# Performance work log

Hardware: AMD Instinct MI355X
Metric: run time of the kernel (lower is better)

## Reference

```python
import jax, jax.numpy as jnp
import numpy as np

EMBED = 64
HEADS = 2
HDIM = EMBED // HEADS  # 32
IN_FEAT = 256
NODES = 3


def _lin(x, W, b=None):
    y = x @ W.T
    return y + b if b is not None else y


def setup_inputs() -> dict:
    key = jax.random.key(0)
    ks = jax.random.split(key, 24)
    B = 131072
    s = 0.05
    inp = {
        "spatial": jax.random.normal(ks[0], (B, IN_FEAT), jnp.float32),
        "genomic": jax.random.normal(ks[1], (B, IN_FEAT), jnp.float32),
        "temporal": jax.random.normal(ks[2], (B, IN_FEAT), jnp.float32),
        "adj_matrix": jnp.ones((B, NODES, NODES), jnp.float32),
        # modality projections (Linear(256,64))
        "Wsp": jax.random.normal(ks[3], (EMBED, IN_FEAT)) * s,
        "bsp": jnp.zeros((EMBED,)),
        "Wge": jax.random.normal(ks[4], (EMBED, IN_FEAT)) * s,
        "bge": jnp.zeros((EMBED,)),
        "Wtm": jax.random.normal(ks[5], (EMBED, IN_FEAT)) * s,
        "btm": jnp.zeros((EMBED,)),
        # GAT: W Linear(64,64,no bias), attention Linear(2*head_dim=64 -> 1, no bias)
        "gat_W": jax.random.normal(ks[6], (EMBED, EMBED)) * s,
        "gat_a": jax.random.normal(ks[7], (2 * HDIM,)) * s,
        # MultiheadAttention(64, 2)
        "in_w": jax.random.normal(ks[8], (3 * EMBED, EMBED)) * s,
        "in_b": jnp.zeros((3 * EMBED,)),
        "out_w": jax.random.normal(ks[9], (EMBED, EMBED)) * s,
        "out_b": jnp.zeros((EMBED,)),
        # LayerNorm(64)
        "ln_g": jnp.ones((EMBED,)),
        "ln_b": jnp.zeros((EMBED,)),
        # predictor 64->32->16->2
        "p1_w": jax.random.normal(ks[10], (32, EMBED)) * s,
        "p1_b": jnp.zeros((32,)),
        "p2_w": jax.random.normal(ks[11], (16, 32)) * s,
        "p2_b": jnp.zeros((16,)),
        "p3_w": jax.random.normal(ks[12], (2, 16)) * s,
        "p3_b": jnp.zeros((2,)),
    }
    return inp


def reference(spatial, genomic, temporal, adj_matrix,
              Wsp, bsp, Wge, bge, Wtm, btm,
              gat_W, gat_a, in_w, in_b, out_w, out_b,
              ln_g, ln_b, p1_w, p1_b, p2_w, p2_b, p3_w, p3_b):
    # Dropout layers are identity in eval mode.
    B = spatial.shape[0]
    sp = jax.nn.relu(_lin(spatial, Wsp, bsp))   # [B, 64]
    ge = jax.nn.relu(_lin(genomic, Wge, bge))
    tm = jax.nn.relu(_lin(temporal, Wtm, btm))
    x = jnp.stack([sp, ge, tm], axis=1)          # [B, 3, 64]

    # ---- GAT layer (dense attention over 3 nodes, 2 heads) ----
    h = _lin(x, gat_W).reshape(B, NODES, HEADS, HDIM)  # [B,3,H,D]
    # a . concat(h_i, h_j) decomposes into a1.h_i + a2.h_j
    e_i = jnp.einsum('bnhd,d->bnh', h, gat_a[:HDIM])
    e_j = jnp.einsum('bnhd,d->bnh', h, gat_a[HDIM:])
    e = e_i[:, :, None, :] + e_j[:, None, :, :]        # [B,3,3,H]
    e = jnp.where(e > 0, e, 0.2 * e)                    # LeakyReLU(0.2)
    e = jnp.where(adj_matrix[..., None] == 0, -1e9, e)
    alpha = jax.nn.softmax(e, axis=2)                   # softmax over j
    h_out = jnp.einsum('bijh,bjhd->bihd', alpha, h).reshape(B, NODES, EMBED)
    gat_pooled = h_out.mean(axis=1)                     # [B, 64]

    # ---- Cross-modal MHA + residual LayerNorm ----
    qkv = _lin(x, in_w, in_b)                           # [B,3,192]
    q, k, v = jnp.split(qkv, 3, axis=-1)
    def heads(t):
        return t.reshape(B, NODES, HEADS, HDIM).transpose(0, 2, 1, 3)
    q, k, v = heads(q), heads(k), heads(v)              # [B,H,3,D]
    sc = jnp.einsum('bhqd,bhkd->bhqk', q, k) / jnp.sqrt(jnp.float32(HDIM))
    attn = jax.nn.softmax(sc, axis=-1)
    o = jnp.einsum('bhqk,bhkd->bhqd', attn, v).transpose(0, 2, 1, 3).reshape(B, NODES, EMBED)
    attn_out = _lin(o, out_w, out_b)
    y = x + attn_out
    mu = y.mean(-1, keepdims=True)
    var = ((y - mu) ** 2).mean(-1, keepdims=True)
    y = (y - mu) / jnp.sqrt(var + 1e-5) * ln_g + ln_b
    cross_modal = y.mean(axis=1)                        # [B, 64]

    # ---- Predictor ----
    combined = gat_pooled + cross_modal
    z = jax.nn.relu(_lin(combined, p1_w, p1_b))
    z = jax.nn.relu(_lin(z, p2_w, p2_b))
    out = _lin(z, p3_w, p3_b)                           # [B, 2]
    return out[:, 0], out[:, 1]
```

## Files before the change

### kernel.cpp

```cpp
#include <hip/hip_runtime.h>

typedef __attribute__((ext_vector_type(8))) short v8s;
typedef __attribute__((ext_vector_type(4))) float v4f;

#define MFMA16(a, b, c) __builtin_amdgcn_mfma_f32_16x16x32_bf16((a), (b), (c), 0, 0, 0)
#define SCQ 0.17677669529663687f

__device__ __forceinline__ short f2bf(float f) {
    unsigned u = __float_as_uint(f);
    u += 0x7FFFu + ((u >> 16) & 1u);
    return (short)(u >> 16);
}
__device__ __forceinline__ float bf2f(short s) {
    return __uint_as_float(((unsigned)(unsigned short)s) << 16);
}
__device__ __forceinline__ float bfly16(float v) {
#pragma unroll
    for (int m = 1; m < 16; m <<= 1) v += __shfl_xor(v, m);
    return v;
}
__device__ __forceinline__ void gload16(const float* g, float* l) {
    __builtin_amdgcn_global_load_lds((const __attribute__((address_space(1))) void*)g,
                                     (__attribute__((address_space(3))) void*)l, 16, 0, 0);
}

__global__ void giman_prep(const float* __restrict__ Wsp, const float* __restrict__ Wge,
                           const float* __restrict__ Wtm, const float* __restrict__ gatW,
                           const float* __restrict__ gat_a,
                           const float* __restrict__ inw, const float* __restrict__ outw,
                           const float* __restrict__ p1w, const float* __restrict__ p2w,
                           const float* __restrict__ in_b, const float* __restrict__ out_b,
                           short* __restrict__ ws) {
    int idx = blockIdx.x * 256 + threadIdx.x;
    if (idx < 73216) {
        int j = idx & 7, l = (idx >> 3) & 63;
        int lr = l & 15, lc = ((l >> 4) << 3) + j;
        float val;
        if (idx < 49152) {
            const float* W; int off;
            if (idx < 16384)      { W = Wsp; off = idx; }
            else if (idx < 32768) { W = Wge; off = idx - 16384; }
            else                  { W = Wtm; off = idx - 32768; }
            int t = off >> 9, kk = t & 7, nb = t >> 3;
            val = W[(nb * 16 + lr) * 256 + kk * 32 + lc];
        } else if (idx < 54272) {
            int t = (idx - 49152) >> 9, kk = t & 1, nb = t >> 1;
            if (nb < 4) {
                val = gatW[(nb * 16 + lr) * 64 + kk * 32 + lc];
            } else {
                int f = kk * 32 + lc;
                val = 0.f;
                if (lr < 4) {
                    float s = 0.f;
                    for (int d = 0; d < 32; ++d)
                        s += gat_a[(lr >> 1) * 32 + d] * gatW[((lr & 1) * 32 + d) * 64 + f];
                    val = s;
                } else if (lr < 6) {
                    int h = lr - 4;
                    float s = 0.f;
                    for (int d = 0; d < 32; ++d)
                        s += inw[(32 * h + d) * 64 + f] * in_b[64 + 32 * h + d];
                    val = s * SCQ;
                } else if (lr < 8) {
                    int h = lr - 6;
                    float s = 0.f;
                    for (int d = 0; d < 32; ++d)
                        s += inw[(64 + 32 * h + d) * 64 + f] * in_b[32 * h + d];
                    val = s * SCQ;
                }
            }
        } else if (idx < 62464) {
            int t = (idx - 54272) >> 9, kk = t & 1, nbh = t >> 1;
            int h = nbh >> 2, nb = nbh & 3;
            int a = kk * 32 + lc, b = nb * 16 + lr;
            float s = 0.f;
            for (int d = 0; d < 32; ++d)
                s += inw[(32 * h + d) * 64 + a] * inw[(64 + 32 * h + d) * 64 + b];
            val = s * SCQ;
        } else if (idx < 70656) {
            int t = (idx - 62464) >> 9, kk = t & 1, nbh = t >> 1;
            int h = nbh >> 2, nb = nbh & 3;
            int r = nb * 16 + lr, c = kk * 32 + lc;
            float s = 0.f;
            for (int k = 0; k < 32; ++k)
                s += outw[r * 64 + h * 32 + k] * inw[(128 + h * 32 + k) * 64 + c];
            val = s;
        } else if (idx < 72704) {
            int t = (idx - 70656) >> 9, kk = t & 1, nb = t >> 1;
            val = p1w[(nb * 16 + lr) * 64 + kk * 32 + lc];
        } else {
            val = p2w[lr * 32 + lc];
        }
        ws[idx] = f2bf(val);
    } else if (idx < 73280) {
        int r = idx - 73216;
        float s = out_b[r];
        for (int k = 0; k < 64; ++k) s += outw[r * 64 + 128 + k] * in_b[128 + k];
        ((float*)(ws + 73216))[r] = s;
    } else if (idx < 73282) {
        int h = idx - 73280;
        float s = 0.f;
        for (int d = 0; d < 32; ++d) s += in_b[32 * h + d] * in_b[64 + 32 * h + d];
        ((float*)(ws + 73216))[64 + h] = s * SCQ;
    }
}

__global__ __launch_bounds__(256)
void giman_proj(const float* __restrict__ spatial, const float* __restrict__ genomic,
                const float* __restrict__ temporal,
                const float* __restrict__ bsp, const float* __restrict__ bge,
                const float* __restrict__ btm,
                const short* __restrict__ wf, short* __restrict__ xg, int Btot)
{
    __shared__ __align__(16) float xs[32][260];

    const int wv = threadIdx.x >> 6;
    const int lane = threadIdx.x & 63;
    const int lq = lane & 15, lg = lane >> 4;
    const int half = wv & 1;
    const int nbp  = wv >> 1;
    const int nG = Btot >> 5;
    const int nItems = 3 * nG;

    for (int it = blockIdx.x; it < nItems; it += gridDim.x) {
        const int m = it / nG;
        const int g = it - m * nG;
        const int s0 = g * 32;

        const float* Xm = (m == 0 ? spatial : (m == 1 ? genomic : temporal));
        const float* src = Xm + (size_t)s0 * 256;
        const float* Bm = (m == 0 ? bsp : (m == 1 ? bge : btm));
        const v8s* bwf = (const v8s*)(wf + m * 16384);

#pragma unroll
        for (int i = 0; i < 8; ++i) {
            int row = wv * 8 + i;
            gload16(src + row * 256 + lane * 4, &xs[row][0]);
        }
        __syncthreads();

        v4f acc0 = (v4f){0.f, 0.f, 0.f, 0.f};
        v4f acc1 = (v4f){0.f, 0.f, 0.f, 0.f};
#pragma unroll
        for (int kk = 0; kk < 8; ++kk) {
            const float* rp = &xs[half * 16 + lq][kk * 32 + lg * 8];
            float4 u = *(const float4*)rp;
            float4 v = *(const float4*)(rp + 4);
            v8s af;
            af[0] = f2bf(u.x); af[1] = f2bf(u.y); af[2] = f2bf(u.z); af[3] = f2bf(u.w);
            af[4] = f2bf(v.x); af[5] = f2bf(v.y); af[6] = f2bf(v.z); af[7] = f2bf(v.w);
            acc0 = MFMA16(af, bwf[((nbp * 2 + 0) * 8 + kk) * 64 + lane], acc0);
            acc1 = MFMA16(af, bwf[((nbp * 2 + 1) * 8 + kk) * 64 + lane], acc1);
        }

        float bb0 = Bm[nbp * 32 + lq], bb1 = Bm[nbp * 32 + 16 + lq];
#pragma unroll
        for (int r = 0; r < 4; ++r) {
            int row = s0 + half * 16 + 4 * lg + r;
            size_t base = ((size_t)row * 3 + m) * 64 + nbp * 32 + lq;
            float v0 = acc0[r] + bb0; v0 = v0 > 0.f ? v0 : 0.f;
            float v1 = acc1[r] + bb1; v1 = v1 > 0.f ? v1 : 0.f;
            xg[base] = f2bf(v0);
            xg[base + 16] = f2bf(v1);
        }
        __syncthreads();
    }
}

__global__ __launch_bounds__(256)
void giman_main(const float* __restrict__ adj, const short* __restrict__ wf,
                const short* __restrict__ xg,
                const float* __restrict__ ln_g, const float* __restrict__ ln_b,
                const float* __restrict__ p1b, const float* __restrict__ p2b,
                const float* __restrict__ p3w, const float* __restrict__ p3bb,
                float* __restrict__ dout, int Btot)
{
    __shared__ __align__(16) short x_lds[4][48][72];
    __shared__ __align__(16) short v_lds[4][16][72];
    __shared__ __align__(16) float a_lds[4][148];

    const int wv   = threadIdx.x >> 6;
    const int lane = threadIdx.x & 63;
    const int lq   = lane & 15;
    const int lg   = lane >> 4;
    const int grpb = lane & 48;
    const int s0   = blockIdx.x * 64 + wv * 16;
    if (s0 + 16 > Btot) return;

    short (*xw)[72] = x_lds[wv];
    short (*vtr)[72] = v_lds[wv];

    if (lane < 36)
        *(float4*)&a_lds[wv][lane * 4] = *(const float4*)(adj + (size_t)s0 * 9 + lane * 4);

    {
        const short* xsrc = xg + (size_t)s0 * 192;
#pragma unroll
        for (int i = 0; i < 6; ++i) {
            int c = lane + 64 * i;
            v8s val = *(const v8s*)(xsrc + c * 8);
            *(v8s*)&xw[c >> 3][(c & 7) * 8] = val;
        }
    }

    const float* cbp = (const float*)(wf + 73216);
    float cbv[4], lgv[4], lbv[4];
#pragma unroll
    for (int nb = 0; nb < 4; ++nb) {
        int c = nb * 16 + lq;
        cbv[nb] = cbp[c];
        lgv[nb] = ln_g[c];
        lbv[nb] = ln_b[c];
    }
    const float gmv0 = cbp[64], gmv1 = cbp[65];
    const float inv3 = 1.f / 3.f;

    const v8s* gwf = (const v8s*)(wf + 49152);
    const v8s* pff = (const v8s*)(wf + 54272);
    const v8s* uf  = (const v8s*)(wf + 62464);

#pragma unroll 1
    for (int t = 0; t < 4; ++t) {
        int rn = lq & 3; rn = (rn == 3) ? 2 : rn;
        const short* xrp = xw[(t * 4 + (lq >> 2)) * 3 + rn];
        v8s xa0 = *(const v8s*)(xrp + lg * 8);
        v8s xa1 = *(const v8s*)(xrp + 32 + lg * 8);

        float gp[4];
        v4f eacc = (v4f){0.f, 0.f, 0.f, 0.f};
        {
            v4f hacc[4];
#pragma unroll
            for (int nb = 0; nb < 4; ++nb) {
                v4f a = (v4f){0.f, 0.f, 0.f, 0.f};
                a = MFMA16(xa0, gwf[(nb * 2 + 0) * 64 + lane], a);
                a = MFMA16(xa1, gwf[(nb * 2 + 1) * 64 + lane], a);
                hacc[nb] = a;
            }
            eacc = MFMA16(xa0, gwf[8 * 64 + lane], eacc);
            eacc = MFMA16(xa1, gwf[9 * 64 + lane], eacc);

            const float* amp = &a_lds[wv][(t * 4 + lg) * 9];
            float wj0[2], wj1[2], wj2[2];
#pragma unroll
            for (int h = 0; h < 2; ++h) {
                float ei0 = __shfl(eacc[0], grpb + h);
                float ei1 = __shfl(eacc[1], grpb + h);
                float ei2 = __shfl(eacc[2], grpb + h);
                float ej0 = __shfl(eacc[0], grpb + 2 + h);
                float ej1 = __shfl(eacc[1], grpb + 2 + h);
                float ej2 = __shfl(eacc[2], grpb + 2 + h);
                float w0 = 0.f, w1 = 0.f, w2 = 0.f;
#pragma unroll
                for (int i = 0; i < 3; ++i) {
                    float eiv = i == 0 ? ei0 : (i == 1 ? ei1 : ei2);
                    float e0 = eiv + ej0; e0 = e0 > 0.f ? e0 : 0.2f * e0; if (amp[i * 3 + 0] == 0.f) e0 = -1e9f;
                    float e1 = eiv + ej1; e1 = e1 > 0.f ? e1 : 0.2f * e1; if (amp[i * 3 + 1] == 0.f) e1 = -1e9f;
                    float e2 = eiv + ej2; e2 = e2 > 0.f ? e2 : 0.2f * e2; if (amp[i * 3 + 2] == 0.f) e2 = -1e9f;
                    float mx = fmaxf(e0, fmaxf(e1, e2));
                    float q0 = __expf(e0 - mx), q1 = __expf(e1 - mx), q2 = __expf(e2 - mx);
                    float inv = 1.f / (q0 + q1 + q2);
                    w0 += q0 * inv; w1 += q1 * inv; w2 += q2 * inv;
                }
                wj0[h] = w0; wj1[h] = w1; wj2[h] = w2;
            }
#pragma unroll
            for (int nb = 0; nb < 4; ++nb) {
                int h = nb >> 1;
                gp[nb] = (wj0[h] * hacc[nb][0] + wj1[h] * hacc[nb][1] + wj2[h] * hacc[nb][2]) * inv3;
            }
        }

        float y[4][3];
#pragma unroll
        for (int nb = 0; nb < 4; ++nb)
#pragma unroll
            for (int r = 0; r < 3; ++r)
                y[nb][r] = bf2f(xw[(t * 4 + lg) * 3 + r][nb * 16 + lq]) + cbv[nb];

        const int sb = grpb + (grpb >> 2);
#pragma unroll
        for (int h = 0; h < 2; ++h) {
            {
                v4f va[4];
#pragma unroll
                for (int nb = 0; nb < 4; ++nb) {
                    v4f a = (v4f){0.f, 0.f, 0.f, 0.f};
                    a = MFMA16(xa0, pff[((h * 4 + nb) * 2 + 0) * 64 + lane], a);
                    a = MFMA16(xa1, pff[((h * 4 + nb) * 2 + 1) * 64 + lane], a);
                    va[nb] = a;
                }
#pragma unroll
                for (int nb = 0; nb < 4; ++nb)
#pragma unroll
                    for (int r = 0; r < 3; ++r)
                        vtr[lg * 4 + r][nb * 16 + lq] = f2bf(va[nb][r]);
            }
            v8s aq0 = *(const v8s*)&vtr[lq][lg * 8];
            v8s aq1 = *(const v8s*)&vtr[lq][32 + lg * 8];
            v4f S = (v4f){0.f, 0.f, 0.f, 0.f};
            S = MFMA16(aq0, xa0, S);
            S = MFMA16(aq1, xa1, S);

            float alh[9];
            {
                float gm = h ? gmv1 : gmv0;
                float bv0 = __shfl(eacc[0], grpb + 6 + h) + gm;
                float bv1 = __shfl(eacc[1], grpb + 6 + h) + gm;
                float bv2 = __shfl(eacc[2], grpb + 6 + h) + gm;
#pragma unroll
                for (int i = 0; i < 3; ++i) {
                    float av = __shfl(eacc[i], grpb + 4 + h);
                    float e0 = __shfl(S[i], sb + 0) + av + bv0;
                    float e1 = __shfl(S[i], sb + 1) + av + bv1;
                    float e2 = __shfl(S[i], sb + 2) + av + bv2;
                    float mx = fmaxf(e0, fmaxf(e1, e2));
                    float w0 = __expf(e0 - mx), w1 = __expf(e1 - mx), w2 = __expf(e2 - mx);
                    float inv = 1.f / (w0 + w1 + w2);
                    alh[i * 3 + 0] = w0 * inv;
                    alh[i * 3 + 1] = w1 * inv;
                    alh[i * 3 + 2] = w2 * inv;
                }
            }

#pragma unroll
            for (int nb = 0; nb < 4; ++nb) {
                v4f u = (v4f){0.f, 0.f, 0.f, 0.f};
                u = MFMA16(xa0, uf[((h * 4 + nb) * 2 + 0) * 64 + lane], u);
                u = MFMA16(xa1, uf[((h * 4 + nb) * 2 + 1) * 64 + lane], u);
#pragma unroll
                for (int r = 0; r < 3; ++r)
                    y[nb][r] += alh[r * 3 + 0] * u[0] + alh[r * 3 + 1] * u[1]
                              + alh[r * 3 + 2] * u[2];
            }
        }

        float mu[3], rs[3];
#pragma unroll
        for (int r = 0; r < 3; ++r) {
            float sm = y[0][r] + y[1][r] + y[2][r] + y[3][r];
            float sq = y[0][r] * y[0][r] + y[1][r] * y[1][r]
                     + y[2][r] * y[2][r] + y[3][r] * y[3][r];
            sm = bfly16(sm); sq = bfly16(sq);
            float m_ = sm * (1.f / 64.f);
            float var = sq * (1.f / 64.f) - m_ * m_;
            mu[r] = m_;
            rs[r] = rsqrtf(var + 1e-5f);
        }
#pragma unroll
        for (int nb = 0; nb < 4; ++nb) {
            float cm = (y[nb][0] - mu[0]) * rs[0] + (y[nb][1] - mu[1]) * rs[1]
                     + (y[nb][2] - mu[2]) * rs[2];
            float comb = gp[nb] + cm * inv3 * lgv[nb] + lbv[nb];
            xw[t * 4 + lg][nb * 16 + lq] = f2bf(comb);
        }
    }

    {
        const v8s* p1f = (const v8s*)(wf + 70656);
        const v8s* p2f = (const v8s*)(wf + 72704);
        short (*zw)[40] = (short (*)[40])(&xw[16][0]);
        const short* crp = &xw[lq][0];
        v8s ca0 = *(const v8s*)(crp + lg * 8);
        v8s ca1 = *(const v8s*)(crp + 32 + lg * 8);
        const float pb1v0 = p1b[lq], pb1v1 = p1b[16 + lq], pb2v = p2b[lq];
        const float p3w0 = p3w[lq], p3w1 = p3w[16 + lq];
        v4f z1[2];
#pragma unroll
        for (int nb = 0; nb < 2; ++nb) {
            float bb = nb ? pb1v1 : pb1v0;
            v4f a = (v4f){bb, bb, bb, bb};
            a = MFMA16(ca0, p1f[(nb * 2 + 0) * 64 + lane], a);
            a = MFMA16(ca1, p1f[(nb * 2 + 1) * 64 + lane], a);
            z1[nb] = a;
        }
#pragma unroll
        for (int nb = 0; nb < 2; ++nb)
#pragma unroll
            for (int r = 0; r < 4; ++r) {
                float v = z1[nb][r];
                v = v > 0.f ? v : 0.f;
                zw[lg * 4 + r][nb * 16 + lq] = f2bf(v);
            }
        v8s za = *(const v8s*)(&zw[lq][0] + lg * 8);
        v4f z2 = (v4f){pb2v, pb2v, pb2v, pb2v};
        z2 = MFMA16(za, p2f[lane], z2);
        const float p3b0 = p3bb[0], p3b1 = p3bb[1];
#pragma unroll
        for (int r = 0; r < 4; ++r) {
            float v = z2[r];
            v = v > 0.f ? v : 0.f;
            float po0 = bfly16(v * p3w0);
            float po1 = bfly16(v * p3w1);
            if (lq == 0) {
                dout[s0 + lg * 4 + r] = po0 + p3b0;
                dout[Btot + s0 + lg * 4 + r] = po1 + p3b1;
            }
        }
    }
}

extern "C" void kernel_launch(void* const* d_in, const int* in_sizes, int n_in,
                              void* d_out, int out_size, void* d_ws, size_t ws_size,
                              hipStream_t stream) {
    const float* spatial  = (const float*)d_in[0];
    const float* genomic  = (const float*)d_in[1];
    const float* temporal = (const float*)d_in[2];
    const float* adj      = (const float*)d_in[3];
    const float* Wsp = (const float*)d_in[4];
    const float* bsp = (const float*)d_in[5];
    const float* Wge = (const float*)d_in[6];
    const float* bge = (const float*)d_in[7];
    const float* Wtm = (const float*)d_in[8];
    const float* btm = (const float*)d_in[9];
    const float* gatW  = (const float*)d_in[10];
    const float* gat_a = (const float*)d_in[11];
    const float* in_w  = (const float*)d_in[12];
    const float* in_b  = (const float*)d_in[13];
    const float* out_w = (const float*)d_in[14];
    const float* out_b = (const float*)d_in[15];
    const float* ln_g  = (const float*)d_in[16];
    const float* ln_b  = (const float*)d_in[17];
    const float* p1w = (const float*)d_in[18];
    const float* p1b = (const float*)d_in[19];
    const float* p2w = (const float*)d_in[20];
    const float* p2b = (const float*)d_in[21];
    const float* p3w = (const float*)d_in[22];
    const float* p3b = (const float*)d_in[23];
    float* out = (float*)d_out;
    const int Btot = in_sizes[0] / 256;

    short* wf = (short*)d_ws;
    short* xg = wf + 81920;

    giman_prep<<<(73282 + 255) / 256, 256, 0, stream>>>(Wsp, Wge, Wtm, gatW, gat_a,
                                                        in_w, out_w, p1w, p2w,
                                                        in_b, out_b, wf);
    giman_proj<<<1024, 256, 0, stream>>>(spatial, genomic, temporal,
                                         bsp, bge, btm, wf, xg, Btot);
    giman_main<<<Btot / 64, 256, 0, stream>>>(adj, wf, xg,
                                              ln_g, ln_b, p1b, p2b, p3w, p3b,
                                              out, Btot);
}
```

Measured before the change: 221.3 us.

## Double-buffer projection input loads with async LDS prefetch and per-modality grid

The projection kernel now processes 16-row tiles with double-buffered LDS, issuing the global-to-LDS loads for the next tile before computing the current one and using explicit vmcnt waits instead of full syncs. Each block is pinned to one modality through blockIdx.y, and each wave computes one 16-column output block instead of two. The grid becomes 342x3 blocks. The aim is to hide HBM latency on a bandwidth-bound projection, at the cost of fragile hand-counted waitcnt logic and less MFMA work per wave.

```diff
diff --git a/kernel.cpp b/kernel.cpp
--- a/kernel.cpp
+++ b/kernel.cpp
@@ -112,58 +112,64 @@
                 const float* __restrict__ btm,
                 const short* __restrict__ wf, short* __restrict__ xg, int Btot)
 {
-    __shared__ __align__(16) float xs[32][260];
+    __shared__ __align__(16) float xs[2][16][260];
 
     const int wv = threadIdx.x >> 6;
     const int lane = threadIdx.x & 63;
     const int lq = lane & 15, lg = lane >> 4;
-    const int half = wv & 1;
-    const int nbp  = wv >> 1;
-    const int nG = Btot >> 5;
-    const int nItems = 3 * nG;
-
-    for (int it = blockIdx.x; it < nItems; it += gridDim.x) {
-        const int m = it / nG;
-        const int g = it - m * nG;
-        const int s0 = g * 32;
-
-        const float* Xm = (m == 0 ? spatial : (m == 1 ? genomic : temporal));
-        const float* src = Xm + (size_t)s0 * 256;
-        const float* Bm = (m == 0 ? bsp : (m == 1 ? bge : btm));
-        const v8s* bwf = (const v8s*)(wf + m * 16384);
-
-#pragma unroll
-        for (int i = 0; i < 8; ++i) {
-            int row = wv * 8 + i;
-            gload16(src + row * 256 + lane * 4, &xs[row][0]);
-        }
-        __syncthreads();
-
-        v4f acc0 = (v4f){0.f, 0.f, 0.f, 0.f};
-        v4f acc1 = (v4f){0.f, 0.f, 0.f, 0.f};
+    const int m = blockIdx.y;
+    const int nG = Btot >> 4;
+
+    const float* Xm = (m == 0 ? spatial : (m == 1 ? genomic : temporal));
+    const float* Bm = (m == 0 ? bsp : (m == 1 ? bge : btm));
+    const v8s* bwf = (const v8s*)(wf + m * 16384);
+    const float bb = Bm[wv * 16 + lq];
+
+    const int g0 = blockIdx.x;
+    const int nit = (nG - g0 + gridDim.x - 1) / gridDim.x;
+
+    {
+        const float* src = Xm + (size_t)g0 * 16 * 256;
+#pragma unroll
+        for (int i = 0; i < 4; ++i)
+            gload16(src + (wv * 4 + i) * 256 + lane * 4, &xs[0][wv * 4 + i][0]);
+    }
+
+    for (int it = 0; it < nit; ++it) {
+        const int cur = it & 1;
+        if (it + 1 < nit) {
+            const float* src = Xm + ((size_t)g0 + (size_t)(it + 1) * gridDim.x) * 16 * 256;
+#pragma unroll
+            for (int i = 0; i < 4; ++i)
+                gload16(src + (wv * 4 + i) * 256 + lane * 4, &xs[cur ^ 1][wv * 4 + i][0]);
+            if (it == 0) { asm volatile("s_waitcnt vmcnt(4)" ::: "memory"); }
+            else         { asm volatile("s_waitcnt vmcnt(8)" ::: "memory"); }
+        } else {
+            asm volatile("s_waitcnt vmcnt(4)" ::: "memory");
+        }
+        __builtin_amdgcn_sched_barrier(0);
+        __builtin_amdgcn_s_barrier();
+
+        v4f acc = (v4f){0.f, 0.f, 0.f, 0.f};
 #pragma unroll
         for (int kk = 0; kk < 8; ++kk) {
-            const float* rp = &xs[half * 16 + lq][kk * 32 + lg * 8];
+            const float* rp = &xs[cur][lq][kk * 32 + lg * 8];
             float4 u = *(const float4*)rp;
             float4 v = *(const float4*)(rp + 4);
             v8s af;
             af[0] = f2bf(u.x); af[1] = f2bf(u.y); af[2] = f2bf(u.z); af[3] = f2bf(u.w);
             af[4] = f2bf(v.x); af[5] = f2bf(v.y); af[6] = f2bf(v.z); af[7] = f2bf(v.w);
-            acc0 = MFMA16(af, bwf[((nbp * 2 + 0) * 8 + kk) * 64 + lane], acc0);
-            acc1 = MFMA16(af, bwf[((nbp * 2 + 1) * 8 + kk) * 64 + lane], acc1);
-        }
-
-        float bb0 = Bm[nbp * 32 + lq], bb1 = Bm[nbp * 32 + 16 + lq];
+            acc = MFMA16(af, bwf[(wv * 8 + kk) * 64 + lane], acc);
+        }
+
+        const int s0 = (g0 + it * gridDim.x) * 16;
 #pragma unroll
         for (int r = 0; r < 4; ++r) {
-            int row = s0 + half * 16 + 4 * lg + r;
-            size_t base = ((size_t)row * 3 + m) * 64 + nbp * 32 + lq;
-            float v0 = acc0[r] + bb0; v0 = v0 > 0.f ? v0 : 0.f;
-            float v1 = acc1[r] + bb1; v1 = v1 > 0.f ? v1 : 0.f;
-            xg[base] = f2bf(v0);
-            xg[base + 16] = f2bf(v1);
-        }
-        __syncthreads();
+            float v = acc[r] + bb;
+            v = v > 0.f ? v : 0.f;
+            xg[((size_t)(s0 + 4 * lg + r) * 3 + m) * 64 + wv * 16 + lq] = f2bf(v);
+        }
+        __builtin_amdgcn_s_barrier();
     }
 }
 
@@ -436,8 +442,9 @@
     giman_prep<<<(73282 + 255) / 256, 256, 0, stream>>>(Wsp, Wge, Wtm, gatW, gat_a,
                                                         in_w, out_w, p1w, p2w,
                                                         in_b, out_b, wf);
-    giman_proj<<<1024, 256, 0, stream>>>(spatial, genomic, temporal,
-                                         bsp, bge, btm, wf, xg, Btot);
+    dim3 pg(342, 3);
+    giman_proj<<<pg, 256, 0, stream>>>(spatial, genomic, temporal,
+                                       bsp, bge, btm, wf, xg, Btot);
     giman_main<<<Btot / 64, 256, 0, stream>>>(adj, wf, xg,
                                               ln_g, ln_b, p1b, p2b, p3w, p3b,
                                               out, Btot);
```

Result: slower. 241.9 us (+9.3%).
